# Optimization experiments

Measured on AMD Instinct MI355X. Metric: run time of the kernel, lower is better.

## Reference

```python
import jax, jax.numpy as jnp
import numpy as np
import math

EMBED = 1024
HEADS = 16
HEAD_DIM = 64
HIDDEN = 4 * EMBED
EPS = 1e-5


def setup_inputs() -> dict:
    key = jax.random.key(0)
    ks = jax.random.split(key, 12)
    B, T, C = 2, 2048, EMBED
    s = 0.02
    return {
        "x": jax.random.normal(ks[0], (B, T, C), jnp.float32),
        "ln1_g": jnp.ones((C,), jnp.float32),
        "ln1_b": jnp.zeros((C,), jnp.float32),
        "qkv_w": jax.random.normal(ks[1], (C, 3 * C), jnp.float32) * s,
        "qkv_b": jnp.zeros((3 * C,), jnp.float32),
        "out_w": jax.random.normal(ks[2], (C, C), jnp.float32) * s,
        "out_b": jnp.zeros((C,), jnp.float32),
        "ln2_g": jnp.ones((C,), jnp.float32),
        "ln2_b": jnp.zeros((C,), jnp.float32),
        "fc1_w": jax.random.normal(ks[3], (C, HIDDEN), jnp.float32) * s,
        "fc1_b": jnp.zeros((HIDDEN,), jnp.float32),
        "fc2_w": jax.random.normal(ks[4], (HIDDEN, C), jnp.float32) * s,
        "fc2_b": jnp.zeros((C,), jnp.float32),
    }


def _layernorm(x, g, b):
    mu = jnp.mean(x, axis=-1, keepdims=True)
    var = jnp.var(x, axis=-1, keepdims=True)
    return (x - mu) * jax.lax.rsqrt(var + EPS) * g + b


def _attention(x, qkv_w, qkv_b, out_w, out_b):
    B, T, C = x.shape
    qkv = x @ qkv_w + qkv_b  # [B,T,3C]
    q, k, v = jnp.split(qkv, 3, axis=-1)
    # [B,H,T,hd]
    def heads(t):
        return t.reshape(B, T, HEADS, HEAD_DIM).transpose(0, 2, 1, 3)
    q, k, v = heads(q), heads(k), heads(v)
    scale = 1.0 / math.sqrt(HEAD_DIM)
    attn = jnp.einsum('bhqd,bhkd->bhqk', q, k) * scale
    causal = jnp.triu(jnp.ones((T, T), bool), k=1)
    attn = jnp.where(causal, -jnp.inf, attn)
    attn = jax.nn.softmax(attn, axis=-1)
    out = jnp.einsum('bhqk,bhkd->bhqd', attn, v)
    out = out.transpose(0, 2, 1, 3).reshape(B, T, C)
    return out @ out_w + out_b


def reference(x, ln1_g, ln1_b, qkv_w, qkv_b, out_w, out_b, ln2_g, ln2_b, fc1_w, fc1_b, fc2_w, fc2_b):
    x = x + _attention(_layernorm(x, ln1_g, ln1_b), qkv_w, qkv_b, out_w, out_b)
    h = _layernorm(x, ln2_g, ln2_b)
    h = jax.nn.gelu(h @ fc1_w + fc1_b, approximate=False) @ fc2_w + fc2_b
    return x + h
```

## Files before the change

### kernel.cpp

```cpp
#include <hip/hip_runtime.h>
#include <hip/hip_bf16.h>
#include <math.h>

typedef float f32x4 __attribute__((ext_vector_type(4)));
typedef __bf16 bf16x8 __attribute__((ext_vector_type(8)));
typedef __hip_bfloat16 bf16;

constexpr int T_SEQ = 2048;
constexpr int C_EMB = 1024;
constexpr int N_HEAD = 16;
constexpr int D_HEAD = 64;
constexpr int BATCH = 2;
constexpr int M_ROWS = BATCH * T_SEQ;
constexpr int HIDDEN_DIM = 4096;

static __device__ __forceinline__ f32x4 zero4() {
  f32x4 z; z[0] = 0.f; z[1] = 0.f; z[2] = 0.f; z[3] = 0.f; return z;
}

static __device__ __forceinline__ void gl_lds16(const bf16* g, bf16* l) {
  __builtin_amdgcn_global_load_lds(
      (const __attribute__((address_space(1))) unsigned int*)g,
      (__attribute__((address_space(3))) unsigned int*)l, 16, 0, 0);
}

static __device__ __forceinline__ int swz_row(int l) {
  return 2 * (l >> 3) + (((l >> 2) ^ (l >> 5)) & 1);
}
static __device__ __forceinline__ int swz_col16(int l) {
  return (l & 3) ^ ((l >> 3) & 3);
}
static __device__ __forceinline__ int swz_rd(int rr, int g) {
  return (rr >> 1) * 64 + ((((rr & 1) ^ ((rr >> 3) & 1))) << 5) +
         (((g ^ ((rr >> 1) & 3)) & 3) << 3);
}

__global__ __launch_bounds__(256) void ln_kernel(const float* __restrict__ x,
                                                 const float* __restrict__ gamma,
                                                 const float* __restrict__ beta,
                                                 bf16* __restrict__ out) {
  int row = blockIdx.x;
  const float* xr = x + (size_t)row * C_EMB;
  int t = threadIdx.x;
  float4 v = *(const float4*)&xr[t * 4];
  float s = v.x + v.y + v.z + v.w;
  float ss = v.x * v.x + v.y * v.y + v.z * v.z + v.w * v.w;
#pragma unroll
  for (int off = 32; off > 0; off >>= 1) {
    s += __shfl_down(s, off, 64);
    ss += __shfl_down(ss, off, 64);
  }
  __shared__ float sbuf[8];
  int w = t >> 6;
  if ((t & 63) == 0) { sbuf[w] = s; sbuf[4 + w] = ss; }
  __syncthreads();
  s = sbuf[0] + sbuf[1] + sbuf[2] + sbuf[3];
  ss = sbuf[4] + sbuf[5] + sbuf[6] + sbuf[7];
  float mu = s * (1.0f / C_EMB);
  float var = ss * (1.0f / C_EMB) - mu * mu;
  float rstd = rsqrtf(var + 1e-5f);
  float4 g4 = *(const float4*)&gamma[t * 4];
  float4 b4 = *(const float4*)&beta[t * 4];
  bf16* orow = out + (size_t)row * C_EMB + t * 4;
  orow[0] = __float2bfloat16((v.x - mu) * rstd * g4.x + b4.x);
  orow[1] = __float2bfloat16((v.y - mu) * rstd * g4.y + b4.y);
  orow[2] = __float2bfloat16((v.z - mu) * rstd * g4.z + b4.z);
  orow[3] = __float2bfloat16((v.w - mu) * rstd * g4.w + b4.w);
}

__global__ __launch_bounds__(256) void cast_transpose(const float* __restrict__ src,
                                                      bf16* __restrict__ dst,
                                                      int K, int N) {
  __shared__ float tile[32][33];
  int n0 = blockIdx.x * 32, k0 = blockIdx.y * 32;
  int tx = threadIdx.x & 31, ty = threadIdx.x >> 5;
#pragma unroll
  for (int i = 0; i < 4; ++i)
    tile[ty + 8 * i][tx] = src[(size_t)(k0 + ty + 8 * i) * N + n0 + tx];
  __syncthreads();
#pragma unroll
  for (int i = 0; i < 4; ++i)
    dst[(size_t)(n0 + ty + 8 * i) * K + k0 + tx] = __float2bfloat16(tile[tx][ty + 8 * i]);
}

__global__ __launch_bounds__(256) void transpose_v(const bf16* __restrict__ V,
                                                   bf16* __restrict__ Vt) {
  int tt = blockIdx.x, bh = blockIdx.y;
  __shared__ bf16 tile[64][72];
  const bf16* src = V + ((size_t)bh * T_SEQ + tt * 64) * 64;
  int t = threadIdx.x;
  for (int idx = t; idx < 512; idx += 256) {
    int r = idx >> 3, c = (idx & 7) * 8;
    *(int4*)&tile[r][c] = *(const int4*)&src[r * 64 + c];
  }
  __syncthreads();
  bf16* dst = Vt + ((size_t)bh * 64) * T_SEQ + tt * 64;
  for (int idx = t; idx < 512; idx += 256) {
    int d = idx >> 3, c = (idx & 7) * 8;
    union { bf16 h[8]; int4 v; } u;
#pragma unroll
    for (int j = 0; j < 8; ++j) u.h[j] = tile[c + j][d];
    *(int4*)&dst[(size_t)d * T_SEQ + c] = u.v;
  }
}

template <int EPI>
__global__ __launch_bounds__(256) void gemm128(
    const bf16* __restrict__ A, const bf16* __restrict__ Bt,
    const float* __restrict__ bias, int M, int N, int K, int ksplit,
    float* __restrict__ out_f32, const float* __restrict__ res,
    bf16* __restrict__ out_b16,
    bf16* __restrict__ q_out, bf16* __restrict__ k_out, bf16* __restrict__ v_out,
    float* __restrict__ part0, float* __restrict__ part1) {
  __shared__ bf16 Alds[128 * 32];
  __shared__ bf16 Blds[128 * 32];

  int gx = gridDim.x, nwg = gx * gridDim.y;
  int flat = blockIdx.y * gx + blockIdx.x;
  int swz = (flat & 7) * (nwg >> 3) + (flat >> 3);
  int bx = swz % gx, by = swz / gx;

  int m0 = by * 128, n0 = bx * 128;
  int t = threadIdx.x;
  int w = t >> 6, lane = t & 63, g = lane >> 4, r16 = lane & 15;
  int w_m = (w >> 1) * 64, w_n = (w & 1) * 64;

  f32x4 acc[4][4];
#pragma unroll
  for (int i = 0; i < 4; ++i)
#pragma unroll
    for (int j = 0; j < 4; ++j) acc[i][j] = zero4();

  int srow = swz_row(lane);
  int scol = swz_col16(lane) * 8;

  int klen = K / ksplit;
  int kbeg = blockIdx.z * klen, kend = kbeg + klen;

  for (int k0 = kbeg; k0 < kend; k0 += 32) {
    __syncthreads();
#pragma unroll
    for (int p = 0; p < 2; ++p) {
      int chunk = w * 2 + p;
      const bf16* ga = A + (size_t)(m0 + chunk * 16 + srow) * K + k0 + scol;
      const bf16* gb = Bt + (size_t)(n0 + chunk * 16 + srow) * K + k0 + scol;
      gl_lds16(ga, &Alds[chunk * 512]);
      gl_lds16(gb, &Blds[chunk * 512]);
    }
    __syncthreads();
    bf16x8 af[4], bfr[4];
#pragma unroll
    for (int mi = 0; mi < 4; ++mi) {
      int R = w_m + mi * 16 + r16;
      af[mi] = *(const bf16x8*)&Alds[(R >> 4) * 512 + swz_rd(R & 15, g)];
    }
#pragma unroll
    for (int ni = 0; ni < 4; ++ni) {
      int R = w_n + ni * 16 + r16;
      bfr[ni] = *(const bf16x8*)&Blds[(R >> 4) * 512 + swz_rd(R & 15, g)];
    }
#pragma unroll
    for (int mi = 0; mi < 4; ++mi)
#pragma unroll
      for (int ni = 0; ni < 4; ++ni)
        acc[mi][ni] = __builtin_amdgcn_mfma_f32_16x16x32_bf16(af[mi], bfr[ni], acc[mi][ni], 0, 0, 0);
  }

  float* pout = (EPI == 3) ? (blockIdx.z == 0 ? part0 : part1) : out_f32;

#pragma unroll
  for (int mi = 0; mi < 4; ++mi) {
#pragma unroll
    for (int ni = 0; ni < 4; ++ni) {
      int col = n0 + w_n + ni * 16 + r16;
      float bv = (EPI == 3) ? 0.0f : bias[col];
#pragma unroll
      for (int reg = 0; reg < 4; ++reg) {
        int row = m0 + w_m + mi * 16 + g * 4 + reg;
        float v = acc[mi][ni][reg] + bv;
        if constexpr (EPI == 0) {
          int part = col >> 10, cc = col & 1023;
          int hh = cc >> 6, dd = cc & 63;
          int bb = row >> 11, tt = row & 2047;
          size_t idx = (((size_t)bb * N_HEAD + hh) * T_SEQ + tt) * D_HEAD + dd;
          if (part == 0) q_out[idx] = __float2bfloat16(v * 0.125f);
          else if (part == 1) k_out[idx] = __float2bfloat16(v);
          else v_out[idx] = __float2bfloat16(v);
        } else if constexpr (EPI == 1) {
          size_t idx = (size_t)row * N + col;
          out_f32[idx] = v + res[idx];
        } else if constexpr (EPI == 2) {
          float ge = 0.5f * v * (1.0f + erff(v * 0.70710678118f));
          out_b16[(size_t)row * N + col] = __float2bfloat16(ge);
        } else {
          pout[(size_t)row * N + col] = v;
        }
      }
    }
  }
}

__global__ __launch_bounds__(256) void reduce_add(const float* __restrict__ p0,
                                                  const float* __restrict__ p1,
                                                  const float* __restrict__ bias,
                                                  const float* __restrict__ res,
                                                  float* __restrict__ out,
                                                  int total, int N) {
  for (int i = (blockIdx.x * 256 + threadIdx.x) * 4; i < total; i += gridDim.x * 1024) {
    float4 a = *(const float4*)&p0[i];
    float4 b = *(const float4*)&p1[i];
    float4 r = *(const float4*)&res[i];
    float4 bi = *(const float4*)&bias[i & (N - 1)];
    float4 o;
    o.x = a.x + b.x + r.x + bi.x;
    o.y = a.y + b.y + r.y + bi.y;
    o.z = a.z + b.z + r.z + bi.z;
    o.w = a.w + b.w + r.w + bi.w;
    *(float4*)&out[i] = o;
  }
}

__global__ __launch_bounds__(256) void attn_kernel(const bf16* __restrict__ Q,
                                                   const bf16* __restrict__ Kg,
                                                   const bf16* __restrict__ Vt,
                                                   bf16* __restrict__ O) {
  constexpr int NQ = T_SEQ / 64;
  int p = blockIdx.x, bh = blockIdx.y;
  int qtA = p, qtB = NQ - 1 - p;
  int b = bh >> 4, h = bh & 15;
  __shared__ bf16 Ks[64 * 64];
  __shared__ bf16 Vs[64 * 64];
  __shared__ bf16 Ps[4][16 * 64];
  int t = threadIdx.x, w = t >> 6, lane = t & 63, g = lane >> 4, r16 = lane & 15;

  const bf16* QpA = Q + ((size_t)bh * T_SEQ + qtA * 64) * 64;
  const bf16* QpB = Q + ((size_t)bh * T_SEQ + qtB * 64) * 64;
  bf16x8 qfA[2], qfB[2];
#pragma unroll
  for (int kk = 0; kk < 2; ++kk) {
    qfA[kk] = *(const bf16x8*)&QpA[(w * 16 + r16) * 64 + kk * 32 + g * 8];
    qfB[kk] = *(const bf16x8*)&QpB[(w * 16 + r16) * 64 + kk * 32 + g * 8];
  }

  float lsA[4] = {0.f, 0.f, 0.f, 0.f}, lsB[4] = {0.f, 0.f, 0.f, 0.f};
  f32x4 oA[4], oB[4];
#pragma unroll
  for (int i = 0; i < 4; ++i) { oA[i] = zero4(); oB[i] = zero4(); }

  bf16* Psw = Ps[w];
  int rowsw = (g * 4) & 7;

  auto process = [&](const bf16x8* qf, float* ls, f32x4* o_acc, bool diag) {
    f32x4 s[4];
#pragma unroll
    for (int ni = 0; ni < 4; ++ni) {
      s[ni] = zero4();
#pragma unroll
      for (int kk = 0; kk < 2; ++kk) {
        bf16x8 kf = *(const bf16x8*)&Ks[(ni * 16 + r16) * 64 + (((kk * 4 + g) ^ (r16 & 7)) << 3)];
        s[ni] = __builtin_amdgcn_mfma_f32_16x16x32_bf16(qf[kk], kf, s[ni], 0, 0, 0);
      }
    }
    if (diag) {
#pragma unroll
      for (int ni = 0; ni < 4; ++ni) {
        int kl = ni * 16 + r16;
#pragma unroll
        for (int reg = 0; reg < 4; ++reg) {
          int ql = w * 16 + g * 4 + reg;
          if (kl > ql) s[ni][reg] = -1e30f;
        }
      }
    }
#pragma unroll
    for (int ni = 0; ni < 4; ++ni) {
#pragma unroll
      for (int reg = 0; reg < 4; ++reg) {
        float pv = __expf(s[ni][reg]);
        s[ni][reg] = pv;
        ls[reg] += pv;
        int rr = g * 4 + reg;
        Psw[rr * 64 + (((ni * 2 + (r16 >> 3)) ^ (rr & 7)) << 3) + (r16 & 7)] =
            __float2bfloat16(pv);
      }
    }
    bf16x8 pf[2];
#pragma unroll
    for (int kk = 0; kk < 2; ++kk)
      pf[kk] = *(const bf16x8*)&Psw[r16 * 64 + (((kk * 4 + g) ^ (r16 & 7)) << 3)];
#pragma unroll
    for (int nd = 0; nd < 4; ++nd)
#pragma unroll
      for (int kk = 0; kk < 2; ++kk) {
        bf16x8 vf = *(const bf16x8*)&Vs[(nd * 16 + r16) * 64 + (((kk * 4 + g) ^ (r16 & 7)) << 3)];
        o_acc[nd] = __builtin_amdgcn_mfma_f32_16x16x32_bf16(pf[kk], vf, o_acc[nd], 0, 0, 0);
      }
  };
  (void)rowsw;

  for (int kt = 0; kt <= qtB; ++kt) {
    __syncthreads();
    const bf16* Kp = Kg + ((size_t)bh * T_SEQ + kt * 64) * 64;
    const bf16* Vp = Vt + (size_t)bh * 64 * T_SEQ + kt * 64;
#pragma unroll
    for (int j = 0; j < 2; ++j) {
      int gidx = w * 128 + j * 64 + lane;
      int r = gidx >> 3, c = (gidx & 7) ^ (r & 7);
      gl_lds16(Kp + r * 64 + c * 8, &Ks[(w * 128 + j * 64) * 8]);
      gl_lds16(Vp + (size_t)r * T_SEQ + c * 8, &Vs[(w * 128 + j * 64) * 8]);
    }
    __syncthreads();
    process(qfB, lsB, oB, kt == qtB);
    if (kt <= qtA) process(qfA, lsA, oA, kt == qtA);
  }

#pragma unroll
  for (int reg = 0; reg < 4; ++reg) {
#pragma unroll
    for (int off = 1; off < 16; off <<= 1) {
      lsA[reg] += __shfl_xor(lsA[reg], off, 64);
      lsB[reg] += __shfl_xor(lsB[reg], off, 64);
    }
  }
#pragma unroll
  for (int reg = 0; reg < 4; ++reg) {
    float invA = 1.0f / lsA[reg];
    float invB = 1.0f / lsB[reg];
    int rowA = b * T_SEQ + qtA * 64 + w * 16 + g * 4 + reg;
    int rowB = b * T_SEQ + qtB * 64 + w * 16 + g * 4 + reg;
#pragma unroll
    for (int nd = 0; nd < 4; ++nd) {
      int col = h * 64 + nd * 16 + r16;
      O[(size_t)rowA * C_EMB + col] = __float2bfloat16(oA[nd][reg] * invA);
      O[(size_t)rowB * C_EMB + col] = __float2bfloat16(oB[nd][reg] * invB);
    }
  }
}

extern "C" void kernel_launch(void* const* d_in, const int* in_sizes, int n_in,
                              void* d_out, int out_size, void* d_ws, size_t ws_size,
                              hipStream_t stream) {
  (void)in_sizes; (void)n_in; (void)out_size; (void)ws_size;
  const float* x     = (const float*)d_in[0];
  const float* ln1_g = (const float*)d_in[1];
  const float* ln1_b = (const float*)d_in[2];
  const float* qkv_w = (const float*)d_in[3];
  const float* qkv_b = (const float*)d_in[4];
  const float* out_w = (const float*)d_in[5];
  const float* out_b = (const float*)d_in[6];
  const float* ln2_g = (const float*)d_in[7];
  const float* ln2_b = (const float*)d_in[8];
  const float* fc1_w = (const float*)d_in[9];
  const float* fc1_b = (const float*)d_in[10];
  const float* fc2_w = (const float*)d_in[11];
  const float* fc2_b = (const float*)d_in[12];
  float* out = (float*)d_out;

  char* ws = (char*)d_ws;
  size_t off = 0;
  auto alloc = [&](size_t bytes) {
    void* p = ws + off;
    off += (bytes + 255) & ~(size_t)255;
    return p;
  };
  bf16* Wqkv = (bf16*)alloc((size_t)3 * C_EMB * C_EMB * 2);
  bf16* Wout = (bf16*)alloc((size_t)C_EMB * C_EMB * 2);
  bf16* W1   = (bf16*)alloc((size_t)HIDDEN_DIM * C_EMB * 2);
  bf16* W2   = (bf16*)alloc((size_t)C_EMB * HIDDEN_DIM * 2);
  float* x2  = (float*)alloc((size_t)M_ROWS * C_EMB * 4);
  bf16* Xb   = (bf16*)alloc((size_t)M_ROWS * C_EMB * 2);
  bf16* Qb   = (bf16*)alloc((size_t)M_ROWS * C_EMB * 2 * 4);
  bf16* Kb   = Qb + (size_t)M_ROWS * C_EMB;
  bf16* Vb   = Kb + (size_t)M_ROWS * C_EMB;
  bf16* Vtb  = Vb + (size_t)M_ROWS * C_EMB;
  bf16* H1   = Qb;
  float* p0o = (float*)Qb;
  float* p1o = (float*)Vb;
  float* p0f = (float*)Wqkv;
  float* p1f = (float*)alloc((size_t)M_ROWS * C_EMB * 4);

  cast_transpose<<<dim3(3 * C_EMB / 32, C_EMB / 32), 256, 0, stream>>>(qkv_w, Wqkv, C_EMB, 3 * C_EMB);
  cast_transpose<<<dim3(C_EMB / 32, C_EMB / 32), 256, 0, stream>>>(out_w, Wout, C_EMB, C_EMB);
  cast_transpose<<<dim3(HIDDEN_DIM / 32, C_EMB / 32), 256, 0, stream>>>(fc1_w, W1, C_EMB, HIDDEN_DIM);
  cast_transpose<<<dim3(C_EMB / 32, HIDDEN_DIM / 32), 256, 0, stream>>>(fc2_w, W2, HIDDEN_DIM, C_EMB);

  ln_kernel<<<M_ROWS, 256, 0, stream>>>(x, ln1_g, ln1_b, Xb);

  gemm128<0><<<dim3(3 * C_EMB / 128, M_ROWS / 128), 256, 0, stream>>>(
      Xb, Wqkv, qkv_b, M_ROWS, 3 * C_EMB, C_EMB, 1,
      nullptr, nullptr, nullptr, Qb, Kb, Vb, nullptr, nullptr);

  transpose_v<<<dim3(T_SEQ / 64, BATCH * N_HEAD), 256, 0, stream>>>(Vb, Vtb);

  attn_kernel<<<dim3(T_SEQ / 128, BATCH * N_HEAD), 256, 0, stream>>>(Qb, Kb, Vtb, Xb);

  gemm128<3><<<dim3(C_EMB / 128, M_ROWS / 128, 2), 256, 0, stream>>>(
      Xb, Wout, nullptr, M_ROWS, C_EMB, C_EMB, 2,
      nullptr, nullptr, nullptr, nullptr, nullptr, nullptr, p0o, p1o);
  reduce_add<<<2048, 256, 0, stream>>>(p0o, p1o, out_b, x, x2,
                                       M_ROWS * C_EMB, C_EMB);

  ln_kernel<<<M_ROWS, 256, 0, stream>>>(x2, ln2_g, ln2_b, Xb);

  gemm128<2><<<dim3(HIDDEN_DIM / 128, M_ROWS / 128), 256, 0, stream>>>(
      Xb, W1, fc1_b, M_ROWS, HIDDEN_DIM, C_EMB, 1,
      nullptr, nullptr, H1, nullptr, nullptr, nullptr, nullptr, nullptr);

  gemm128<3><<<dim3(C_EMB / 128, M_ROWS / 128, 2), 256, 0, stream>>>(
      H1, W2, nullptr, M_ROWS, C_EMB, HIDDEN_DIM, 2,
      nullptr, nullptr, nullptr, nullptr, nullptr, nullptr, p0f, p1f);
  reduce_add<<<2048, 256, 0, stream>>>(p0f, p1f, fc2_b, x2, out,
                                       M_ROWS * C_EMB, C_EMB);
}
```

Baseline: 286.9 us.

## Double-buffer LDS tiles in GEMM and attention kernels with one barrier per step

Both the GEMM and the attention kernel now keep two LDS buffers for the operand tiles. The next K-slice (or K/V tile) is issued with async global-to-LDS loads before the MFMA work on the current buffer, and each iteration ends with a single barrier instead of two. The GEMM also precomputes its swizzled LDS read offsets and global pointers outside the loop. The aim is to hide global load latency behind compute and halve barrier count, at the cost of doubling LDS per workgroup, which may reduce occupancy.

```diff
diff --git a/kernel.cpp b/kernel.cpp
--- a/kernel.cpp
+++ b/kernel.cpp
@@ -112,8 +112,8 @@
     bf16* __restrict__ out_b16,
     bf16* __restrict__ q_out, bf16* __restrict__ k_out, bf16* __restrict__ v_out,
     float* __restrict__ part0, float* __restrict__ part1) {
-  __shared__ bf16 Alds[128 * 32];
-  __shared__ bf16 Blds[128 * 32];
+  __shared__ bf16 Alds[2][128 * 32];
+  __shared__ bf16 Blds[2][128 * 32];
 
   int gx = gridDim.x, nwg = gx * gridDim.y;
   int flat = blockIdx.y * gx + blockIdx.x;
@@ -133,37 +133,57 @@
 
   int srow = swz_row(lane);
   int scol = swz_col16(lane) * 8;
+  int chunk0 = w * 2, chunk1 = w * 2 + 1;
 
   int klen = K / ksplit;
-  int kbeg = blockIdx.z * klen, kend = kbeg + klen;
-
-  for (int k0 = kbeg; k0 < kend; k0 += 32) {
-    __syncthreads();
-#pragma unroll
-    for (int p = 0; p < 2; ++p) {
-      int chunk = w * 2 + p;
-      const bf16* ga = A + (size_t)(m0 + chunk * 16 + srow) * K + k0 + scol;
-      const bf16* gb = Bt + (size_t)(n0 + chunk * 16 + srow) * K + k0 + scol;
-      gl_lds16(ga, &Alds[chunk * 512]);
-      gl_lds16(gb, &Blds[chunk * 512]);
-    }
-    __syncthreads();
+  int kbeg = blockIdx.z * klen;
+  int NT = klen / 32;
+
+  const bf16* gA0 = A + (size_t)(m0 + chunk0 * 16 + srow) * K + kbeg + scol;
+  const bf16* gA1 = A + (size_t)(m0 + chunk1 * 16 + srow) * K + kbeg + scol;
+  const bf16* gB0 = Bt + (size_t)(n0 + chunk0 * 16 + srow) * K + kbeg + scol;
+  const bf16* gB1 = Bt + (size_t)(n0 + chunk1 * 16 + srow) * K + kbeg + scol;
+
+  int offA[4], offB[4];
+#pragma unroll
+  for (int mi = 0; mi < 4; ++mi) {
+    int R = w_m + mi * 16 + r16;
+    offA[mi] = (R >> 4) * 512 + swz_rd(R & 15, g);
+  }
+#pragma unroll
+  for (int ni = 0; ni < 4; ++ni) {
+    int R = w_n + ni * 16 + r16;
+    offB[ni] = (R >> 4) * 512 + swz_rd(R & 15, g);
+  }
+
+  gl_lds16(gA0, &Alds[0][chunk0 * 512]); gA0 += 32;
+  gl_lds16(gA1, &Alds[0][chunk1 * 512]); gA1 += 32;
+  gl_lds16(gB0, &Blds[0][chunk0 * 512]); gB0 += 32;
+  gl_lds16(gB1, &Blds[0][chunk1 * 512]); gB1 += 32;
+  __syncthreads();
+
+  for (int tt = 0; tt < NT; ++tt) {
+    int cur = tt & 1;
+    if (tt + 1 < NT) {
+      int nxt = cur ^ 1;
+      gl_lds16(gA0, &Alds[nxt][chunk0 * 512]); gA0 += 32;
+      gl_lds16(gA1, &Alds[nxt][chunk1 * 512]); gA1 += 32;
+      gl_lds16(gB0, &Blds[nxt][chunk0 * 512]); gB0 += 32;
+      gl_lds16(gB1, &Blds[nxt][chunk1 * 512]); gB1 += 32;
+    }
     bf16x8 af[4], bfr[4];
 #pragma unroll
-    for (int mi = 0; mi < 4; ++mi) {
-      int R = w_m + mi * 16 + r16;
-      af[mi] = *(const bf16x8*)&Alds[(R >> 4) * 512 + swz_rd(R & 15, g)];
-    }
-#pragma unroll
-    for (int ni = 0; ni < 4; ++ni) {
-      int R = w_n + ni * 16 + r16;
-      bfr[ni] = *(const bf16x8*)&Blds[(R >> 4) * 512 + swz_rd(R & 15, g)];
-    }
+    for (int mi = 0; mi < 4; ++mi)
+      af[mi] = *(const bf16x8*)&Alds[cur][offA[mi]];
+#pragma unroll
+    for (int ni = 0; ni < 4; ++ni)
+      bfr[ni] = *(const bf16x8*)&Blds[cur][offB[ni]];
 #pragma unroll
     for (int mi = 0; mi < 4; ++mi)
 #pragma unroll
       for (int ni = 0; ni < 4; ++ni)
         acc[mi][ni] = __builtin_amdgcn_mfma_f32_16x16x32_bf16(af[mi], bfr[ni], acc[mi][ni], 0, 0, 0);
+    __syncthreads();
   }
 
   float* pout = (EPI == 3) ? (blockIdx.z == 0 ? part0 : part1) : out_f32;
@@ -181,8 +201,8 @@
         if constexpr (EPI == 0) {
           int part = col >> 10, cc = col & 1023;
           int hh = cc >> 6, dd = cc & 63;
-          int bb = row >> 11, tt = row & 2047;
-          size_t idx = (((size_t)bb * N_HEAD + hh) * T_SEQ + tt) * D_HEAD + dd;
+          int bb = row >> 11, tt2 = row & 2047;
+          size_t idx = (((size_t)bb * N_HEAD + hh) * T_SEQ + tt2) * D_HEAD + dd;
           if (part == 0) q_out[idx] = __float2bfloat16(v * 0.125f);
           else if (part == 1) k_out[idx] = __float2bfloat16(v);
           else v_out[idx] = __float2bfloat16(v);
@@ -228,8 +248,8 @@
   int p = blockIdx.x, bh = blockIdx.y;
   int qtA = p, qtB = NQ - 1 - p;
   int b = bh >> 4, h = bh & 15;
-  __shared__ bf16 Ks[64 * 64];
-  __shared__ bf16 Vs[64 * 64];
+  __shared__ bf16 Ks[2][64 * 64];
+  __shared__ bf16 Vs[2][64 * 64];
   __shared__ bf16 Ps[4][16 * 64];
   int t = threadIdx.x, w = t >> 6, lane = t & 63, g = lane >> 4, r16 = lane & 15;
 
@@ -248,16 +268,29 @@
   for (int i = 0; i < 4; ++i) { oA[i] = zero4(); oB[i] = zero4(); }
 
   bf16* Psw = Ps[w];
-  int rowsw = (g * 4) & 7;
-
-  auto process = [&](const bf16x8* qf, float* ls, f32x4* o_acc, bool diag) {
+
+  int sg0 = w * 128 + lane, sg1 = w * 128 + 64 + lane;
+  int sr0 = sg0 >> 3, sc0 = (sg0 & 7) ^ (sr0 & 7);
+  int sr1 = sg1 >> 3, sc1 = (sg1 & 7) ^ (sr1 & 7);
+
+  auto stage = [&](int kt, int buf) {
+    const bf16* Kp = Kg + ((size_t)bh * T_SEQ + kt * 64) * 64;
+    const bf16* Vp = Vt + (size_t)bh * 64 * T_SEQ + kt * 64;
+    gl_lds16(Kp + sr0 * 64 + sc0 * 8, &Ks[buf][(w * 128) * 8]);
+    gl_lds16(Vp + (size_t)sr0 * T_SEQ + sc0 * 8, &Vs[buf][(w * 128) * 8]);
+    gl_lds16(Kp + sr1 * 64 + sc1 * 8, &Ks[buf][(w * 128 + 64) * 8]);
+    gl_lds16(Vp + (size_t)sr1 * T_SEQ + sc1 * 8, &Vs[buf][(w * 128 + 64) * 8]);
+  };
+
+  auto process = [&](const bf16x8* qf, float* ls, f32x4* o_acc, bool diag,
+                     const bf16* Ksb, const bf16* Vsb) {
     f32x4 s[4];
 #pragma unroll
     for (int ni = 0; ni < 4; ++ni) {
       s[ni] = zero4();
 #pragma unroll
       for (int kk = 0; kk < 2; ++kk) {
-        bf16x8 kf = *(const bf16x8*)&Ks[(ni * 16 + r16) * 64 + (((kk * 4 + g) ^ (r16 & 7)) << 3)];
+        bf16x8 kf = *(const bf16x8*)&Ksb[(ni * 16 + r16) * 64 + (((kk * 4 + g) ^ (r16 & 7)) << 3)];
         s[ni] = __builtin_amdgcn_mfma_f32_16x16x32_bf16(qf[kk], kf, s[ni], 0, 0, 0);
       }
     }
@@ -292,26 +325,19 @@
     for (int nd = 0; nd < 4; ++nd)
 #pragma unroll
       for (int kk = 0; kk < 2; ++kk) {
-        bf16x8 vf = *(const bf16x8*)&Vs[(nd * 16 + r16) * 64 + (((kk * 4 + g) ^ (r16 & 7)) << 3)];
+        bf16x8 vf = *(const bf16x8*)&Vsb[(nd * 16 + r16) * 64 + (((kk * 4 + g) ^ (r16 & 7)) << 3)];
         o_acc[nd] = __builtin_amdgcn_mfma_f32_16x16x32_bf16(pf[kk], vf, o_acc[nd], 0, 0, 0);
       }
   };
-  (void)rowsw;
-
+
+  stage(0, 0);
+  __syncthreads();
   for (int kt = 0; kt <= qtB; ++kt) {
+    int cur = kt & 1;
+    if (kt + 1 <= qtB) stage(kt + 1, cur ^ 1);
+    process(qfB, lsB, oB, kt == qtB, &Ks[cur][0], &Vs[cur][0]);
+    if (kt <= qtA) process(qfA, lsA, oA, kt == qtA, &Ks[cur][0], &Vs[cur][0]);
     __syncthreads();
-    const bf16* Kp = Kg + ((size_t)bh * T_SEQ + kt * 64) * 64;
-    const bf16* Vp = Vt + (size_t)bh * 64 * T_SEQ + kt * 64;
-#pragma unroll
-    for (int j = 0; j < 2; ++j) {
-      int gidx = w * 128 + j * 64 + lane;
-      int r = gidx >> 3, c = (gidx & 7) ^ (r & 7);
-      gl_lds16(Kp + r * 64 + c * 8, &Ks[(w * 128 + j * 64) * 8]);
-      gl_lds16(Vp + (size_t)r * T_SEQ + c * 8, &Vs[(w * 128 + j * 64) * 8]);
-    }
-    __syncthreads();
-    process(qfB, lsB, oB, kt == qtB);
-    if (kt <= qtA) process(qfA, lsA, oA, kt == qtA);
   }
 
 #pragma unroll
```

Measured after the change: 268.1 us. 6.5% less time.
